# Kernel optimization log

Hardware: AMD Instinct MI355X
Metric: run time of the kernel (lower is better)

## Reference

```python
import jax, jax.numpy as jnp
import numpy as np
from jax import lax

FS = 44100.0
B, T = 8, 22050
N_CH, LG, LH, M = 31, 2048, 512, 12
F32 = np.float32


def _bp_fir(f1, f2, K, fs):
    # windowed-sinc bandpass FIR, peak-normalized
    t = np.arange(K) - (K - 1) / 2.0
    lp = lambda fc: 2.0 * fc / fs * np.sinc(2.0 * fc / fs * t)
    h = (lp(f2) - lp(f1)) * np.hamming(K)
    return (h / np.abs(np.fft.rfft(h)).max()).astype(F32)


def _gammatone_fir(fs, K, flow, fhigh, n_ch):
    # 4th-order gammatone impulse responses, 1-ERB spaced fc, peak-normalized
    erb = lambda f: 21.4 * np.log10(4.37 * f / 1000.0 + 1.0)
    ierb = lambda e: (10.0 ** (e / 21.4) - 1.0) * 1000.0 / 4.37
    fc = ierb(np.linspace(erb(flow), erb(fhigh), n_ch))
    t = np.arange(K) / fs
    bw = 1.019 * 24.7 * (4.37 * fc / 1000.0 + 1.0)
    g = t[None] ** 3 * np.exp(-2 * np.pi * bw[:, None] * t[None]) * np.cos(2 * np.pi * fc[:, None] * t[None])
    g = g / np.abs(np.fft.rfft(g, axis=1)).max(axis=1, keepdims=True)
    return g.astype(F32)


def setup_inputs():
    key = jax.random.key(0)
    x = jax.random.normal(key, (B, T), dtype=jnp.float32) * 0.01
    return {
        "x": x,
        "hp_fir": jnp.asarray(_bp_fir(50.0, 16000.0, LH, FS)),   # headphone/outer ear
        "me_fir": jnp.asarray(_bp_fir(450.0, 8500.0, LH, FS)),   # middle ear
        "gt_fir": jnp.asarray(_gammatone_fir(FS, LG, 80.0, 8000.0, N_CH)),
    }


def _conv_causal(x, h):
    # x: [B, Cin, T]; h: [Cout, Cin, K]. Kernel flipped so this is true FIR convolution, causal padding.
    K = h.shape[-1]
    return lax.conv_general_dilated(x, h[:, :, ::-1], (1,), [(K - 1, 0)],
                                    dimension_numbers=("NCH", "OIH", "NCH"))


def _forward(x, hp_fir, me_fir, gt_fir):
    # Stage 0a/0b: headphone + middle-ear FIR
    y = _conv_causal(x[:, None, :], hp_fir[None, None, :])
    y = _conv_causal(y, me_fir[None, None, :])
    # Stage 1: gammatone filterbank -> [B, N, T]
    y = _conv_causal(y, gt_fir[:, None, :])
    bsz, nch, _ = y.shape

    # Stage 2: IHC envelope (breebaart2001): halfwave rectify + 5 cascaded one-pole LP @ 2 kHz
    hw = jnp.maximum(y, 0.0)
    a_lp = jnp.float32(np.exp(-2.0 * np.pi * 2000.0 / FS))

    def ihc_step(s, xt):  # s: [5, B, N], xt: [B, N]
        s0 = a_lp * s[0] + (1.0 - a_lp) * xt
        s1 = a_lp * s[1] + (1.0 - a_lp) * s0
        s2 = a_lp * s[2] + (1.0 - a_lp) * s1
        s3 = a_lp * s[3] + (1.0 - a_lp) * s2
        s4 = a_lp * s[4] + (1.0 - a_lp) * s3
        return jnp.stack([s0, s1, s2, s3, s4]), s4

    _, env = lax.scan(ihc_step, jnp.zeros((5, bsz, nch), jnp.float32), jnp.moveaxis(hw, -1, 0))  # env: [T,B,N]

    # Stage 3: adaptation loops (5 loops, osses2021 limit=5)
    minlvl = jnp.float32(1e-5)
    taus = np.array([0.005, 0.05, 0.129, 0.253, 0.5], F32)
    a1 = jnp.asarray(np.exp(-1.0 / (FS * taus)).astype(F32))
    b0 = 1.0 - a1
    init = np.float32(1e-5) ** (2.0 ** -np.arange(1, 6, dtype=F32))  # sqrt chain of minlvl
    limit = np.float32(5.0)
    maxv = (1.0 - init ** 2) * limit - 1.0
    factor = jnp.asarray(2.0 * maxv)
    expfac = jnp.asarray(-2.0 / maxv)
    offset = jnp.asarray(maxv - 1.0)
    state0 = jnp.broadcast_to(jnp.asarray(init)[:, None, None], (5, bsz, nch)).astype(jnp.float32)

    def adapt_step(state, xt):  # state: [5, B, N]
        tmp = jnp.maximum(xt, minlvl)
        new = []
        for j in range(5):
            tmp = tmp / state[j]
            limited = factor[j] / (1.0 + jnp.exp(expfac[j] * (tmp - 1.0))) - offset[j]
            tmp = jnp.where(tmp > 1.0, limited, tmp)
            new.append(a1[j] * state[j] + b0[j] * tmp)
        return jnp.stack(new), tmp

    _, ad = lax.scan(adapt_step, state0, env)  # ad: [T, B, N]
    corr = np.float32(1e-5) ** np.float32(2.0 ** -5)
    ad = (ad - corr) * (100.0 / (1.0 - corr))  # model units (MU)

    # Stage 4: modulation filterbank (jepsen2008-style): M complex one-pole resonators (Q=2),
    # real part for mfc<=10 Hz, 1/sqrt(2)-attenuated envelope above.
    mfc = jnp.asarray(np.array([2.5, 5.0, 10.0, 16.7, 27.8, 46.3, 77.2,
                                128.6, 214.3, 357.2, 595.4, 992.3], F32))
    r = jnp.exp(-jnp.pi * (mfc / 2.0) / FS)
    pole = (r * jnp.exp(1j * 2.0 * jnp.pi * mfc / FS)).astype(jnp.complex64)
    b0m = (1.0 - r).astype(jnp.complex64)
    att = jnp.float32(1.0 / np.sqrt(2.0))
    lowband = mfc <= 10.0

    def mod_step(s, xt):  # s: [B, N, M] complex, xt: [B, N]
        s = pole * s + b0m * xt[..., None]
        out = jnp.where(lowband, s.real, att * jnp.sqrt(s.real ** 2 + s.imag ** 2 + 1e-12))
        return s, out

    _, mo = lax.scan(mod_step, jnp.zeros((bsz, nch, M), jnp.complex64), ad)  # mo: [T, B, N, M]
    return jnp.moveaxis(mo, 0, -1)  # [B, N, M, T]


def reference(x, hp_fir, me_fir, gt_fir):
    return _forward(x, hp_fir, me_fir, gt_fir)
```

## Files before the change

kernel.cpp:

```cpp
#include <hip/hip_runtime.h>
#include <math.h>

#define FS_   44100.0
#define B_    8
#define T_    22050
#define NCH   31
#define LG    2048
#define LH    512
#define MM    12
#define BN    248

#define H1LEN 1023

#define C2T   512
#define C2THR 128

#define IHCK  128

#define MODL  441
#define MODC  50

#define NBLK  62
#define TQ    5520
#define ADP   22052

#define OFF_H1    0
#define OFF_G5    1024
#define OFF_X1    1280
#define OFF_HW    177696
#define OFF_AD    OFF_HW
#define OFF_ENV   (OFF_HW + 5468896)
#define OFF_SEND  (OFF_ENV + 5475840)
#define OFF_SINIT (OFF_SEND + 297600)

struct ScanP {
  float a1[5], b0[5], factor[5], efl2[5], offset[5], init[5], rinit[5];
  float minlvl, corr, scale;
};
struct ModP {
  float pre[12], pim[12], pb0[12], pLre[12], pLim[12];
  float att;
};

typedef float f32x4_t __attribute__((ext_vector_type(4)));

__global__ void k_h1(const float* __restrict__ hp, const float* __restrict__ me,
                     float* __restrict__ h1) {
  int k = blockIdx.x * blockDim.x + threadIdx.x;
  if (k >= H1LEN) return;
  int j0 = max(0, k - (LH - 1));
  int j1 = min(LH - 1, k);
  float acc = 0.f;
  for (int j = j0; j <= j1; ++j) acc += hp[j] * me[k - j];
  h1[k] = acc;
}

__global__ void k_g5(float l2a, float c5, float* __restrict__ g5) {
  int k = threadIdx.x;
  float kf = (float)k;
  float binom = (kf + 1.f) * (kf + 2.f) * (kf + 3.f) * (kf + 4.f) * (1.0f / 24.0f);
  g5[k] = c5 * binom * exp2f(kf * l2a);
}

__global__ void k_conv1(const float* __restrict__ x, const float* __restrict__ h1,
                        float* __restrict__ x1) {
  __shared__ float xs[256 + 1022];
  __shared__ float hs[H1LEN];
  int b = blockIdx.y;
  int t0 = blockIdx.x * 256;
  const float* xb = x + b * T_;
  for (int i = threadIdx.x; i < 1278; i += 256) {
    int g = t0 - 1022 + i;
    xs[i] = (g >= 0 && g < T_) ? xb[g] : 0.f;
  }
  for (int i = threadIdx.x; i < H1LEN; i += 256) hs[i] = h1[i];
  __syncthreads();
  int t = t0 + threadIdx.x;
  if (t >= T_) return;
  float acc = 0.f;
  for (int k = 0; k < H1LEN; ++k) acc = fmaf(hs[k], xs[threadIdx.x + 1022 - k], acc);
  x1[b * T_ + t] = acc;
}

__global__ __launch_bounds__(C2THR) void k_conv2(const float* __restrict__ x1,
                                                 const float* __restrict__ gt,
                                                 float* __restrict__ hw) {
  const int H = LG - 1;
  __shared__ __align__(16) float xs[C2T + LG];
  __shared__ __align__(16) float hs[LG];
  int n = blockIdx.y % NCH, b = blockIdx.y / NCH;
  int t0 = blockIdx.x * C2T;
  const float* xb = x1 + b * T_;
  for (int i = threadIdx.x; i < C2T + LG; i += C2THR) {
    int g = t0 - H + i;
    xs[i] = (g >= 0 && g < T_) ? xb[g] : 0.f;
  }
  for (int i = threadIdx.x; i < LG; i += C2THR) hs[i] = gt[n * LG + i];
  __syncthreads();
  int base = threadIdx.x * 4;
  float a0 = 0.f, a1 = 0.f, a2 = 0.f, a3 = 0.f;
  float4 hi = *(const float4*)&xs[base + H + 1];
  for (int k4 = 0; k4 < LG / 4; ++k4) {
    int k = k4 * 4;
    float4 lo = *(const float4*)&xs[base + H - 3 - k];
    float4 hh = *(const float4*)&hs[k];
    a0 = fmaf(hh.x, lo.w, a0); a1 = fmaf(hh.x, hi.x, a1); a2 = fmaf(hh.x, hi.y, a2); a3 = fmaf(hh.x, hi.z, a3);
    a0 = fmaf(hh.y, lo.z, a0); a1 = fmaf(hh.y, lo.w, a1); a2 = fmaf(hh.y, hi.x, a2); a3 = fmaf(hh.y, hi.y, a3);
    a0 = fmaf(hh.z, lo.y, a0); a1 = fmaf(hh.z, lo.z, a1); a2 = fmaf(hh.z, lo.w, a2); a3 = fmaf(hh.z, hi.x, a3);
    a0 = fmaf(hh.w, lo.x, a0); a1 = fmaf(hh.w, lo.y, a1); a2 = fmaf(hh.w, lo.z, a2); a3 = fmaf(hh.w, lo.w, a3);
    hi = lo;
  }
  float* o = hw + (size_t)(b * NCH + n) * T_;
  int t = t0 + base;
  if (t + 0 < T_) o[t + 0] = fmaxf(a0, 0.f);
  if (t + 1 < T_) o[t + 1] = fmaxf(a1, 0.f);
  if (t + 2 < T_) o[t + 2] = fmaxf(a2, 0.f);
  if (t + 3 < T_) o[t + 3] = fmaxf(a3, 0.f);
}

__global__ __launch_bounds__(C2THR) void k_ihc(const float* __restrict__ hw,
                                               const float* __restrict__ g5,
                                               float* __restrict__ env) {
  const int H = IHCK - 1;
  __shared__ __align__(16) float xs[C2T + IHCK];
  __shared__ __align__(16) float hs[IHCK];
  int bn = blockIdx.y;
  int t0 = blockIdx.x * C2T;
  const float* xb = hw + (size_t)bn * T_;
  for (int i = threadIdx.x; i < C2T + IHCK; i += C2THR) {
    int g = t0 - H + i;
    xs[i] = (g >= 0 && g < T_) ? xb[g] : 0.f;
  }
  if (threadIdx.x < IHCK) hs[threadIdx.x] = g5[threadIdx.x];
  __syncthreads();
  int base = threadIdx.x * 4;
  float a0 = 0.f, a1 = 0.f, a2 = 0.f, a3 = 0.f;
  float4 hi = *(const float4*)&xs[base + H + 1];
  for (int k4 = 0; k4 < IHCK / 4; ++k4) {
    int k = k4 * 4;
    float4 lo = *(const float4*)&xs[base + H - 3 - k];
    float4 hh = *(const float4*)&hs[k];
    a0 = fmaf(hh.x, lo.w, a0); a1 = fmaf(hh.x, hi.x, a1); a2 = fmaf(hh.x, hi.y, a2); a3 = fmaf(hh.x, hi.z, a3);
    a0 = fmaf(hh.y, lo.z, a0); a1 = fmaf(hh.y, lo.w, a1); a2 = fmaf(hh.y, hi.x, a2); a3 = fmaf(hh.y, hi.y, a3);
    a0 = fmaf(hh.z, lo.y, a0); a1 = fmaf(hh.z, lo.z, a1); a2 = fmaf(hh.z, lo.w, a2); a3 = fmaf(hh.z, hi.x, a3);
    a0 = fmaf(hh.w, lo.x, a0); a1 = fmaf(hh.w, lo.y, a1); a2 = fmaf(hh.w, lo.z, a2); a3 = fmaf(hh.w, lo.w, a3);
    hi = lo;
  }
  int t = t0 + base;
  if (t < T_) {
    int blk = bn >> 2, s = bn & 3, tq = t >> 2;
    float4* o4 = (float4*)(env + ((size_t)(blk * TQ + tq) * 4 + s) * 4);
    *o4 = make_float4(a0, a1, a2, a3);
  }
}

#define GLD0(DST, PTR)  asm volatile("global_load_dwordx4 %0, %1, off"            : "=v"(DST) : "v"(PTR) : "memory")
#define GLD(DST, PTR, OFFB) \
  asm volatile("global_load_dwordx4 %0, %1, off offset:" #OFFB : "=v"(DST) : "v"(PTR) : "memory")
#define VMWAIT(N) do { asm volatile("s_waitcnt vmcnt(" #N ")" ::: "memory"); \
                       __builtin_amdgcn_sched_barrier(0); } while (0)

__global__ __launch_bounds__(64, 1) void k_scan(const float* __restrict__ env,
                                                float* __restrict__ ad, ScanP p) {
  const int lane = threadIdx.x;
  const int row = lane >> 4, q = lane & 15;
  const int seq = blockIdx.x * 4 + row;
  const bool is4 = (q == 4);
  const float* eb = env + (size_t)blockIdx.x * TQ * 16 + row * 4;
  float* o = ad + (size_t)seq * ADP;

#define SEL5(A) (q==0 ? (A)[0] : q==1 ? (A)[1] : q==2 ? (A)[2] : q==3 ? (A)[3] : (A)[4])
  const float A1  = SEL5(p.a1),   B0  = SEL5(p.b0), FAC = SEL5(p.factor);
  const float EF  = SEL5(p.efl2), NEF = -EF,        NOFF = -SEL5(p.offset);
  float st = SEL5(p.init);
  float r  = SEL5(p.rinit);
#undef SEL5
  const float SC = p.scale, NCS = -p.corr * p.scale, ML = p.minlvl;

  float a1st = A1 * st;
  float tmp = 0.f;
  float o0 = 0.f, o1 = 0.f, o2 = 0.f, o3 = 0.f;

#define BODY(EV)                                                              \
    float evc = fmaxf((EV), ML);                                              \
    float tin = __int_as_float(__builtin_amdgcn_update_dpp(                   \
        __float_as_int(evc), __float_as_int(tmp), 0x111, 0xF, 0xF, false));   \
    float v   = tin * r;                                                      \
    float ex  = __builtin_amdgcn_exp2f(fmaf(EF, v, NEF));                     \
    float lim = fmaf(FAC, __builtin_amdgcn_rcpf(1.0f + ex), NOFF);            \
    tmp = fminf(v, lim);

#define STEP_FILL(EV, K)                                                      \
  { BODY(EV)                                                                  \
    float nst = fmaf(B0, tmp, a1st);                                          \
    st = ((K) >= q) ? nst : st;                                               \
    a1st = A1 * st;                                                           \
    r  = __builtin_amdgcn_rcpf(st); }

#define STEP(EV, OSLOT)                                                       \
  { BODY(EV)                                                                  \
    st = fmaf(B0, tmp, a1st);                                                 \
    a1st = A1 * st;                                                           \
    r  = __builtin_amdgcn_rcpf(st);                                           \
    OSLOT = fmaf(tmp, SC, NCS); }

  f32x4_t bF, b0, b1, b2, b3, b4, b5, b6, b7;
  GLD0(bF, eb);
  GLD(b0, eb, 64);   GLD(b1, eb, 128);  GLD(b2, eb, 192);  GLD(b3, eb, 256);
  GLD(b4, eb, 320);  GLD(b5, eb, 384);  GLD(b6, eb, 448);  GLD(b7, eb, 512);
  VMWAIT(0);

  STEP_FILL(bF.x, 0) STEP_FILL(bF.y, 1) STEP_FILL(bF.z, 2) STEP_FILL(bF.w, 3)

  const float* pld = eb + 9 * 16;
  float* po = o;

#define SUBSTEP(BUF, FOFF, BOFF)                                              \
    VMWAIT(14);                                                               \
    STEP(BUF.x, o0) STEP(BUF.y, o1) STEP(BUF.z, o2) STEP(BUF.w, o3)           \
    if (is4) *(float4*)(po + FOFF) = make_float4(o0, o1, o2, o3);             \
    GLD(BUF, pld, BOFF);

  for (int j = 0; j < 689; ++j) {
    SUBSTEP(b0,  0,   0)
    SUBSTEP(b1,  4,  64)
    SUBSTEP(b2,  8, 128)
    SUBSTEP(b3, 12, 192)
    SUBSTEP(b4, 16, 256)
    SUBSTEP(b5, 20, 320)
    SUBSTEP(b6, 24, 384)
    SUBSTEP(b7, 28, 448)
    pld += 8 * 16;
    po  += 32;
  }
#undef SUBSTEP

  STEP(0.f, o0) STEP(0.f, o1)
  if (is4) *(float4*)(o + 22048) = make_float4(o0, o1, o2, o3);
#undef STEP
#undef STEP_FILL
#undef BODY
}

__global__ void k_modA(const float* __restrict__ ad, float2* __restrict__ send, ModP mp) {
  int id = blockIdx.x * 256 + threadIdx.x;
  if (id >= MODC * BN * MM) return;
  int m = id % MM, bn = (id / MM) % BN, c = id / (MM * BN);
  const float* a = ad + (size_t)bn * ADP + c * MODL;
  float pre = mp.pre[m], pim = mp.pim[m], b0 = mp.pb0[m];
  float sre = 0.f, sim = 0.f;
  for (int i = 0; i < MODL; ++i) {
    float xv = a[i];
    float nre = fmaf(pre, sre, fmaf(-pim, sim, b0 * xv));
    sim = fmaf(pre, sim, pim * sre);
    sre = nre;
  }
  send[id] = make_float2(sre, sim);
}

__global__ void k_modB(const float2* __restrict__ send, float2* __restrict__ sinit, ModP mp) {
  int id = blockIdx.x * blockDim.x + threadIdx.x;
  if (id >= BN * MM) return;
  int m = id % MM;
  float pLre = mp.pLre[m], pLim = mp.pLim[m];
  float Sre = 0.f, Sim = 0.f;
  for (int c = 0; c < MODC; ++c) {
    int idx = c * BN * MM + id;
    sinit[idx] = make_float2(Sre, Sim);
    float2 se = send[idx];
    float nre = pLre * Sre - pLim * Sim + se.x;
    Sim = pLre * Sim + pLim * Sre + se.y;
    Sre = nre;
  }
}

__global__ void k_modC(const float* __restrict__ ad, const float2* __restrict__ sinit,
                       float* __restrict__ out, ModP mp) {
  int id = blockIdx.x * 256 + threadIdx.x;
  if (id >= MODC * BN * MM) return;
  int m = id % MM, bn = (id / MM) % BN, c = id / (MM * BN);
  const float* a = ad + (size_t)bn * ADP + c * MODL;
  float* o = out + ((size_t)bn * MM + m) * T_ + c * MODL;
  float2 s0 = sinit[id];
  float sre = s0.x, sim = s0.y;
  float pre = mp.pre[m], pim = mp.pim[m], b0 = mp.pb0[m], att = mp.att;
  bool low = (m < 3);
  for (int i = 0; i < MODL; ++i) {
    float xv = a[i];
    float nre = fmaf(pre, sre, fmaf(-pim, sim, b0 * xv));
    sim = fmaf(pre, sim, pim * sre);
    sre = nre;
    float mag = att * sqrtf(fmaf(sre, sre, fmaf(sim, sim, 1e-12f)));
    o[i] = low ? sre : mag;
  }
}

extern "C" void kernel_launch(void* const* d_in, const int* in_sizes, int n_in,
                              void* d_out, int out_size, void* d_ws, size_t ws_size,
                              hipStream_t stream) {
  const float* x  = (const float*)d_in[0];
  const float* hp = (const float*)d_in[1];
  const float* me = (const float*)d_in[2];
  const float* gt = (const float*)d_in[3];
  float* ws  = (float*)d_ws;
  float* out = (float*)d_out;

  ScanP sp;
  const double taus[5] = {0.005, 0.05, 0.129, 0.253, 0.5};
  for (int j = 0; j < 5; ++j) {
    double a1 = exp(-1.0 / (FS_ * taus[j]));
    double init = pow(1e-5, pow(2.0, -(double)(j + 1)));
    double maxv = (1.0 - init * init) * 5.0 - 1.0;
    sp.a1[j] = (float)a1;
    sp.b0[j] = (float)(1.0 - a1);
    sp.factor[j] = (float)(2.0 * maxv);
    sp.efl2[j] = (float)(-2.0 / maxv * 1.4426950408889634);
    sp.offset[j] = (float)(maxv - 1.0);
    sp.init[j] = (float)init;
    sp.rinit[j] = (float)(1.0 / init);
  }
  sp.minlvl = 1e-5f;
  double corr = pow(1e-5, pow(2.0, -5.0));
  sp.corr = (float)corr;
  sp.scale = (float)(100.0 / (1.0 - corr));

  ModP mp;
  const double mfc[12] = {2.5, 5.0, 10.0, 16.7, 27.8, 46.3, 77.2, 128.6, 214.3, 357.2, 595.4, 992.3};
  for (int m = 0; m < 12; ++m) {
    double r = exp(-M_PI * (mfc[m] / 2.0) / FS_);
    double th = 2.0 * M_PI * mfc[m] / FS_;
    mp.pre[m] = (float)(r * cos(th));
    mp.pim[m] = (float)(r * sin(th));
    mp.pb0[m] = (float)(1.0 - r);
    double rL = pow(r, (double)MODL);
    mp.pLre[m] = (float)(rL * cos((double)MODL * th));
    mp.pLim[m] = (float)(rL * sin((double)MODL * th));
  }
  mp.att = (float)(1.0 / sqrt(2.0));

  double alp = exp(-2.0 * M_PI * 2000.0 / FS_);
  float l2a = (float)(log(alp) * 1.4426950408889634);
  float c5  = (float)pow(1.0 - alp, 5.0);

  float* h1  = ws + OFF_H1;
  float* g5  = ws + OFF_G5;
  float* x1  = ws + OFF_X1;
  float* hw  = ws + OFF_HW;
  float* env = ws + OFF_ENV;
  float* ad  = ws + OFF_AD;
  float2* send  = (float2*)(ws + OFF_SEND);
  float2* sinit = (float2*)(ws + OFF_SINIT);

  k_h1<<<dim3(2), dim3(512), 0, stream>>>(hp, me, h1);
  k_g5<<<dim3(1), dim3(128), 0, stream>>>(l2a, c5, g5);
  k_conv1<<<dim3(87, B_), dim3(256), 0, stream>>>(x, h1, x1);
  k_conv2<<<dim3((T_ + C2T - 1) / C2T, BN), dim3(C2THR), 0, stream>>>(x1, gt, hw);
  k_ihc<<<dim3((T_ + C2T - 1) / C2T, BN), dim3(C2THR), 0, stream>>>(hw, g5, env);
  k_scan<<<dim3(NBLK), dim3(64), 0, stream>>>(env, ad, sp);
  int nmod = MODC * BN * MM;
  k_modA<<<dim3((nmod + 255) / 256), dim3(256), 0, stream>>>(ad, send, mp);
  k_modB<<<dim3((BN * MM + 255) / 256), dim3(256), 0, stream>>>(send, sinit, mp);
  k_modC<<<dim3((nmod + 255) / 256), dim3(256), 0, stream>>>(ad, sinit, out, mp);
}
```

Baseline: 1.828 ms.

## Widen conv2 register tile to 8 outputs, restructure scan stores, unroll mod loops

The gammatone convolution kernel now computes 8 outputs per thread over a 1024-sample tile instead of 4 over 512. This halves the number of shared-memory filter loads per FMA and uses vectorized float2 stores. In the adaptation scan, the exp argument is reassociated so EF*tin can be computed off the rcp dependency chain, and output stores are batched into pairs of float4 every 8 steps with adjusted wait counts. The modulation loops get unroll pragmas. The trade-off is more registers per thread and fewer blocks for conv2, which may reduce occupancy; the changed scan wait counts carry a risk of ordering errors.

```diff
diff --git a/kernel.cpp b/kernel.cpp
--- a/kernel.cpp
+++ b/kernel.cpp
@@ -14,6 +14,7 @@
 
 #define C2T   512
 #define C2THR 128
+#define C2T8  1024
 
 #define IHCK  128
 
@@ -86,36 +87,52 @@
                                                  const float* __restrict__ gt,
                                                  float* __restrict__ hw) {
   const int H = LG - 1;
-  __shared__ __align__(16) float xs[C2T + LG];
+  __shared__ __align__(16) float xs[C2T8 + LG];
   __shared__ __align__(16) float hs[LG];
   int n = blockIdx.y % NCH, b = blockIdx.y / NCH;
-  int t0 = blockIdx.x * C2T;
+  int t0 = blockIdx.x * C2T8;
   const float* xb = x1 + b * T_;
-  for (int i = threadIdx.x; i < C2T + LG; i += C2THR) {
+  for (int i = threadIdx.x; i < C2T8 + LG; i += C2THR) {
     int g = t0 - H + i;
     xs[i] = (g >= 0 && g < T_) ? xb[g] : 0.f;
   }
   for (int i = threadIdx.x; i < LG; i += C2THR) hs[i] = gt[n * LG + i];
   __syncthreads();
-  int base = threadIdx.x * 4;
-  float a0 = 0.f, a1 = 0.f, a2 = 0.f, a3 = 0.f;
-  float4 hi = *(const float4*)&xs[base + H + 1];
+  int base = threadIdx.x * 8;
+  float a0 = 0.f, a1 = 0.f, a2 = 0.f, a3 = 0.f, a4 = 0.f, a5 = 0.f, a6 = 0.f, a7 = 0.f;
+  float4 Bv = *(const float4*)&xs[base + H + 1];
+  float4 Cv = *(const float4*)&xs[base + H + 5];
   for (int k4 = 0; k4 < LG / 4; ++k4) {
     int k = k4 * 4;
-    float4 lo = *(const float4*)&xs[base + H - 3 - k];
+    float4 A  = *(const float4*)&xs[base + H - 3 - k];
     float4 hh = *(const float4*)&hs[k];
-    a0 = fmaf(hh.x, lo.w, a0); a1 = fmaf(hh.x, hi.x, a1); a2 = fmaf(hh.x, hi.y, a2); a3 = fmaf(hh.x, hi.z, a3);
-    a0 = fmaf(hh.y, lo.z, a0); a1 = fmaf(hh.y, lo.w, a1); a2 = fmaf(hh.y, hi.x, a2); a3 = fmaf(hh.y, hi.y, a3);
-    a0 = fmaf(hh.z, lo.y, a0); a1 = fmaf(hh.z, lo.z, a1); a2 = fmaf(hh.z, lo.w, a2); a3 = fmaf(hh.z, hi.x, a3);
-    a0 = fmaf(hh.w, lo.x, a0); a1 = fmaf(hh.w, lo.y, a1); a2 = fmaf(hh.w, lo.z, a2); a3 = fmaf(hh.w, lo.w, a3);
-    hi = lo;
+    a0 = fmaf(hh.x, A.w,  a0); a1 = fmaf(hh.x, Bv.x, a1); a2 = fmaf(hh.x, Bv.y, a2); a3 = fmaf(hh.x, Bv.z, a3);
+    a4 = fmaf(hh.x, Bv.w, a4); a5 = fmaf(hh.x, Cv.x, a5); a6 = fmaf(hh.x, Cv.y, a6); a7 = fmaf(hh.x, Cv.z, a7);
+    a0 = fmaf(hh.y, A.z,  a0); a1 = fmaf(hh.y, A.w,  a1); a2 = fmaf(hh.y, Bv.x, a2); a3 = fmaf(hh.y, Bv.y, a3);
+    a4 = fmaf(hh.y, Bv.z, a4); a5 = fmaf(hh.y, Bv.w, a5); a6 = fmaf(hh.y, Cv.x, a6); a7 = fmaf(hh.y, Cv.y, a7);
+    a0 = fmaf(hh.z, A.y,  a0); a1 = fmaf(hh.z, A.z,  a1); a2 = fmaf(hh.z, A.w,  a2); a3 = fmaf(hh.z, Bv.x, a3);
+    a4 = fmaf(hh.z, Bv.y, a4); a5 = fmaf(hh.z, Bv.z, a5); a6 = fmaf(hh.z, Bv.w, a6); a7 = fmaf(hh.z, Cv.x, a7);
+    a0 = fmaf(hh.w, A.x,  a0); a1 = fmaf(hh.w, A.y,  a1); a2 = fmaf(hh.w, A.z,  a2); a3 = fmaf(hh.w, A.w,  a3);
+    a4 = fmaf(hh.w, Bv.x, a4); a5 = fmaf(hh.w, Bv.y, a5); a6 = fmaf(hh.w, Bv.z, a6); a7 = fmaf(hh.w, Bv.w, a7);
+    Cv = Bv; Bv = A;
   }
   float* o = hw + (size_t)(b * NCH + n) * T_;
   int t = t0 + base;
-  if (t + 0 < T_) o[t + 0] = fmaxf(a0, 0.f);
-  if (t + 1 < T_) o[t + 1] = fmaxf(a1, 0.f);
-  if (t + 2 < T_) o[t + 2] = fmaxf(a2, 0.f);
-  if (t + 3 < T_) o[t + 3] = fmaxf(a3, 0.f);
+  if (t + 7 < T_) {
+    *(float2*)(o + t + 0) = make_float2(fmaxf(a0, 0.f), fmaxf(a1, 0.f));
+    *(float2*)(o + t + 2) = make_float2(fmaxf(a2, 0.f), fmaxf(a3, 0.f));
+    *(float2*)(o + t + 4) = make_float2(fmaxf(a4, 0.f), fmaxf(a5, 0.f));
+    *(float2*)(o + t + 6) = make_float2(fmaxf(a6, 0.f), fmaxf(a7, 0.f));
+  } else {
+    if (t + 0 < T_) o[t + 0] = fmaxf(a0, 0.f);
+    if (t + 1 < T_) o[t + 1] = fmaxf(a1, 0.f);
+    if (t + 2 < T_) o[t + 2] = fmaxf(a2, 0.f);
+    if (t + 3 < T_) o[t + 3] = fmaxf(a3, 0.f);
+    if (t + 4 < T_) o[t + 4] = fmaxf(a4, 0.f);
+    if (t + 5 < T_) o[t + 5] = fmaxf(a5, 0.f);
+    if (t + 6 < T_) o[t + 6] = fmaxf(a6, 0.f);
+    if (t + 7 < T_) o[t + 7] = fmaxf(a7, 0.f);
+  }
 }
 
 __global__ __launch_bounds__(C2THR) void k_ihc(const float* __restrict__ hw,
@@ -179,14 +196,15 @@
 
   float a1st = A1 * st;
   float tmp = 0.f;
-  float o0 = 0.f, o1 = 0.f, o2 = 0.f, o3 = 0.f;
+  float o0 = 0.f, o1 = 0.f, o2 = 0.f, o3 = 0.f, o4 = 0.f, o5 = 0.f, o6 = 0.f, o7 = 0.f;
 
 #define BODY(EV)                                                              \
     float evc = fmaxf((EV), ML);                                              \
     float tin = __int_as_float(__builtin_amdgcn_update_dpp(                   \
         __float_as_int(evc), __float_as_int(tmp), 0x111, 0xF, 0xF, false));   \
+    float eft = EF * tin;                                                     \
     float v   = tin * r;                                                      \
-    float ex  = __builtin_amdgcn_exp2f(fmaf(EF, v, NEF));                     \
+    float ex  = __builtin_amdgcn_exp2f(fmaf(eft, r, NEF));                    \
     float lim = fmaf(FAC, __builtin_amdgcn_rcpf(1.0f + ex), NOFF);            \
     tmp = fminf(v, lim);
 
@@ -215,25 +233,32 @@
   const float* pld = eb + 9 * 16;
   float* po = o;
 
-#define SUBSTEP(BUF, FOFF, BOFF)                                              \
-    VMWAIT(14);                                                               \
+#define SUBSTEP_A(BUF, BOFF)                                                  \
+    VMWAIT(15);                                                               \
     STEP(BUF.x, o0) STEP(BUF.y, o1) STEP(BUF.z, o2) STEP(BUF.w, o3)           \
-    if (is4) *(float4*)(po + FOFF) = make_float4(o0, o1, o2, o3);             \
     GLD(BUF, pld, BOFF);
 
+#define SUBSTEP_B(BUF, FOFF, BOFF)                                            \
+    VMWAIT(13);                                                               \
+    STEP(BUF.x, o4) STEP(BUF.y, o5) STEP(BUF.z, o6) STEP(BUF.w, o7)           \
+    if (is4) { *(float4*)(po + (FOFF))     = make_float4(o0, o1, o2, o3);     \
+               *(float4*)(po + (FOFF) + 4) = make_float4(o4, o5, o6, o7); }   \
+    GLD(BUF, pld, BOFF);
+
   for (int j = 0; j < 689; ++j) {
-    SUBSTEP(b0,  0,   0)
-    SUBSTEP(b1,  4,  64)
-    SUBSTEP(b2,  8, 128)
-    SUBSTEP(b3, 12, 192)
-    SUBSTEP(b4, 16, 256)
-    SUBSTEP(b5, 20, 320)
-    SUBSTEP(b6, 24, 384)
-    SUBSTEP(b7, 28, 448)
+    SUBSTEP_A(b0, 0)
+    SUBSTEP_B(b1, 0, 64)
+    SUBSTEP_A(b2, 128)
+    SUBSTEP_B(b3, 8, 192)
+    SUBSTEP_A(b4, 256)
+    SUBSTEP_B(b5, 16, 320)
+    SUBSTEP_A(b6, 384)
+    SUBSTEP_B(b7, 24, 448)
     pld += 8 * 16;
     po  += 32;
   }
-#undef SUBSTEP
+#undef SUBSTEP_A
+#undef SUBSTEP_B
 
   STEP(0.f, o0) STEP(0.f, o1)
   if (is4) *(float4*)(o + 22048) = make_float4(o0, o1, o2, o3);
@@ -249,6 +274,7 @@
   const float* a = ad + (size_t)bn * ADP + c * MODL;
   float pre = mp.pre[m], pim = mp.pim[m], b0 = mp.pb0[m];
   float sre = 0.f, sim = 0.f;
+#pragma unroll 4
   for (int i = 0; i < MODL; ++i) {
     float xv = a[i];
     float nre = fmaf(pre, sre, fmaf(-pim, sim, b0 * xv));
@@ -285,6 +311,7 @@
   float sre = s0.x, sim = s0.y;
   float pre = mp.pre[m], pim = mp.pim[m], b0 = mp.pb0[m], att = mp.att;
   bool low = (m < 3);
+#pragma unroll 4
   for (int i = 0; i < MODL; ++i) {
     float xv = a[i];
     float nre = fmaf(pre, sre, fmaf(-pim, sim, b0 * xv));
@@ -354,7 +381,7 @@
   k_h1<<<dim3(2), dim3(512), 0, stream>>>(hp, me, h1);
   k_g5<<<dim3(1), dim3(128), 0, stream>>>(l2a, c5, g5);
   k_conv1<<<dim3(87, B_), dim3(256), 0, stream>>>(x, h1, x1);
-  k_conv2<<<dim3((T_ + C2T - 1) / C2T, BN), dim3(C2THR), 0, stream>>>(x1, gt, hw);
+  k_conv2<<<dim3((T_ + C2T8 - 1) / C2T8, BN), dim3(C2THR), 0, stream>>>(x1, gt, hw);
   k_ihc<<<dim3((T_ + C2T - 1) / C2T, BN), dim3(C2THR), 0, stream>>>(hw, g5, env);
   k_scan<<<dim3(NBLK), dim3(64), 0, stream>>>(env, ad, sp);
   int nmod = MODC * BN * MM;
```

New measurement: 1.910 ms. +4.5%, slower.
